# Kernel tuning notes

Measured on AMD Instinct MI355X. Metric: run time of the kernel, lower is better.

The kernel has to match this reference:

```python
import jax, jax.numpy as jnp
import numpy as np
import math

NHEAD = 8
IOU_THR = 0.2
COS_THR = 0.2


def _build_mask(segments, q):
    # segments: [bz, Lq, 2] (center, length); q: [bz, Lq, d]
    c, l = segments[..., 0], segments[..., 1]
    s, e = c - l / 2, c + l / 2  # ml2se: midpoint-length -> start-end
    inter = jnp.clip(jnp.minimum(e[:, :, None], e[:, None, :])
                     - jnp.maximum(s[:, :, None], s[:, None, :]), 0.0)
    union = l[:, :, None] + l[:, None, :] - inter
    iou = inter / union  # [bz, Lq, Lq]
    qn = q / jnp.maximum(jnp.linalg.norm(q, axis=-1, keepdims=True), 1e-8)
    cos = jnp.einsum('bid,bjd->bij', qn, qn)
    Lq = q.shape[1]
    adj = jnp.broadcast_to(jnp.eye(Lq, dtype=bool), iou.shape)
    adj = jnp.where(iou <= IOU_THR, True, adj)   # adj_matrix[iou<=0.2]=1
    adj = jnp.where(cos <= COS_THR, False, adj)  # adj_matrix[cos<=0.2]=0
    return ~adj  # True = masked


def setup_inputs() -> dict:
    key = jax.random.key(0)
    ks = jax.random.split(key, 8)
    Lq, bz, d = 1024, 8, 512
    bound = 1.0 / math.sqrt(d)
    query = jax.random.normal(ks[0], (Lq, bz, d), jnp.float32)
    segments = jax.random.uniform(ks[1], (bz, Lq, 2), jnp.float32)
    Wq = jax.random.uniform(ks[2], (d, d), jnp.float32, -bound, bound)
    bq = jax.random.uniform(ks[3], (d,), jnp.float32, -bound, bound)
    Wk = jax.random.uniform(ks[4], (d, d), jnp.float32, -bound, bound)
    bk = jax.random.uniform(ks[5], (d,), jnp.float32, -bound, bound)
    Wv = jax.random.uniform(ks[6], (d, d), jnp.float32, -bound, bound)
    bv = jax.random.uniform(ks[7], (d,), jnp.float32, -bound, bound)
    return dict(query=query, segments=segments, Wq=Wq, bq=bq, Wk=Wk, bk=bk,
                Wv=Wv, bv=bv)


def reference(query, segments, Wq, bq, Wk, bk, Wv, bv):
    Lq, bz, d = query.shape
    dh = d // NHEAD
    h = jnp.transpose(query, (1, 0, 2))  # [bz, Lq, d]
    mask = _build_mask(segments, h)      # [bz, Lq, Lq], bool
    Q = (h @ Wq.T + bq).reshape(bz, Lq, NHEAD, dh)
    K = (h @ Wk.T + bk).reshape(bz, Lq, NHEAD, dh)
    V = (h @ Wv.T + bv).reshape(bz, Lq, NHEAD, dh)
    scores = jnp.einsum('bihd,bjhd->bhij', Q, K) / math.sqrt(dh)
    scores = jnp.where(mask[:, None, :, :], -jnp.inf, scores)
    attn = jax.nn.softmax(scores, axis=-1)
    out = jnp.einsum('bhij,bjhd->bihd', attn, V).reshape(bz, Lq, d) + h
    return jnp.transpose(out, (1, 0, 2))  # [Lq, bz, d]
```

## Files before the change

### kernel.cpp

```cpp
#include <hip/hip_runtime.h>
#include <math.h>

#define LQ 1024
#define BZ 8
#define D  512
#define NH 8
#define DH 64
#define IOU_THR 0.2f
#define COS_THR 0.2f
#define NEG (-1e30f)
#define FIXCAP 16384

typedef short bf16x8 __attribute__((ext_vector_type(8)));
typedef float f32x4  __attribute__((ext_vector_type(4)));

#define MFMA16(a, b, cacc) __builtin_amdgcn_mfma_f32_16x16x32_bf16(a, b, cacc, 0, 0, 0)

__device__ inline unsigned short f2bf(float x) {
    union { float f; unsigned int u; } v; v.f = x;
    unsigned int r = v.u + 0x7FFF + ((v.u >> 16) & 1);
    return (unsigned short)(r >> 16);
}

__device__ __forceinline__ void gll16(const void* g, void* ldsbase) {
    __builtin_amdgcn_global_load_lds(
        (const __attribute__((address_space(1))) unsigned int*)g,
        (__attribute__((address_space(3))) unsigned int*)ldsbase, 16, 0, 0);
}

__global__ __launch_bounds__(256) void prep_kernel(const float* __restrict__ query,
                                                   float* __restrict__ h,
                                                   unsigned short* __restrict__ hi,
                                                   float* __restrict__ rnorm) {
    int blk = blockIdx.x;
    int b = blk >> 10, i = blk & 1023;
    const float* src = query + ((size_t)i * BZ + b) * D;
    int tid = threadIdx.x;
    float2 v = ((const float2*)src)[tid];
    ((float2*)(h + (size_t)blk * D))[tid] = v;
    unsigned short hx = f2bf(v.x), hy = f2bf(v.y);
    ((unsigned int*)(hi + (size_t)blk * D))[tid] = (unsigned int)hx | ((unsigned int)hy << 16);
    float ss = v.x * v.x + v.y * v.y;
    __shared__ float red[256];
    red[tid] = ss; __syncthreads();
    for (int s = 128; s > 0; s >>= 1) {
        if (tid < s) red[tid] += red[tid + s];
        __syncthreads();
    }
    if (tid == 0) rnorm[blk] = 1.0f / fmaxf(sqrtf(red[0]), 1e-8f);
}

__global__ __launch_bounds__(256) void cvt_w_kernel(const float* __restrict__ Wq,
                                                    const float* __restrict__ Wk,
                                                    const float* __restrict__ Wv,
                                                    unsigned short* __restrict__ Wb) {
    int t = blockIdx.x * 256 + threadIdx.x;
    int mat = t >> 16;
    int off = (t & 65535) * 4;
    const float* src = (mat == 0) ? Wq : (mat == 1) ? Wk : Wv;
    float4 v = *(const float4*)(src + off);
    uint2 p;
    p.x = (unsigned int)f2bf(v.x) | ((unsigned int)f2bf(v.y) << 16);
    p.y = (unsigned int)f2bf(v.z) | ((unsigned int)f2bf(v.w) << 16);
    *(uint2*)(Wb + (size_t)mat * D * D + off) = p;
}

__global__ __launch_bounds__(256) void mask_kernel(const unsigned short* __restrict__ hi,
                                                   const float* __restrict__ rnorm,
                                                   const float* __restrict__ segments,
                                                   unsigned char* __restrict__ mask,
                                                   unsigned char* __restrict__ summ,
                                                   int* __restrict__ fix_cnt,
                                                   unsigned int* __restrict__ fix_list) {
    __shared__ short As[128 * 64], Bs[128 * 64];
    __shared__ float4 iSE[128], jSE[128];
    __shared__ int summ_lds[8][2];
    int b = blockIdx.z, i0 = blockIdx.y * 128, j0 = blockIdx.x * 128;
    int tid = threadIdx.x, w = tid >> 6, lane = tid & 63;
    int c = lane & 15, q4 = lane >> 4;
    int wr = w >> 1, wc = w & 1;
    if (tid < 16) summ_lds[tid >> 1][tid & 1] = 0;

    f32x4 acc[4][4] = {};
    const char* Asrc = (const char*)(hi + ((size_t)b * LQ + i0) * D);
    const char* Bsrc = (const char*)(hi + ((size_t)b * LQ + j0) * D);

    int rgrp = lane >> 3;
    int qg   = (lane & 7) ^ (rgrp & 7);
    size_t lgoff = (size_t)rgrp * 1024 + (size_t)qg * 16;
    int swz = c & 7;

    for (int k0 = 0; k0 < D; k0 += 64) {
        size_t kb = (size_t)k0 * 2;
        #pragma unroll
        for (int m = 0; m < 4; m++) {
            int n = 4 * w + m;
            gll16(Asrc + kb + (size_t)n * 8192 + lgoff, (char*)As + n * 1024);
            gll16(Bsrc + kb + (size_t)n * 8192 + lgoff, (char*)Bs + n * 1024);
        }
        __syncthreads();
        #pragma unroll
        for (int s = 0; s < 2; s++) {
            bf16x8 af[4], bf[4];
            #pragma unroll
            for (int f = 0; f < 4; f++) {
                af[f] = *(const bf16x8*)&As[(wr * 64 + f * 16 + c) * 64 + ((s * 4 + q4) ^ swz) * 8];
                bf[f] = *(const bf16x8*)&Bs[(wc * 64 + f * 16 + c) * 64 + ((s * 4 + q4) ^ swz) * 8];
            }
            #pragma unroll
            for (int fr = 0; fr < 4; fr++)
                #pragma unroll
                for (int fc = 0; fc < 4; fc++)
                    acc[fr][fc] = MFMA16(af[fr], bf[fc], acc[fr][fc]);
        }
        __syncthreads();
    }

    {
        const float2* seg2 = (const float2*)(segments + (size_t)b * LQ * 2);
        const float* rn = rnorm + b * LQ;
        if (tid < 128) {
            int i = i0 + tid;
            float2 cl = seg2[i];
            iSE[tid] = make_float4(cl.x - cl.y * 0.5f, cl.x + cl.y * 0.5f, cl.y, rn[i]);
        } else {
            int j = j0 + tid - 128;
            float2 cl = seg2[j];
            jSE[tid - 128] = make_float4(cl.x - cl.y * 0.5f, cl.x + cl.y * 0.5f, cl.y, rn[j]);
        }
        __syncthreads();
    }

    unsigned char* mbase = mask + ((size_t)b << 20);
    #pragma unroll
    for (int fr = 0; fr < 4; fr++) {
        int anyun = 0;
        #pragma unroll
        for (int r = 0; r < 4; r++) {
            int il = wr * 64 + fr * 16 + q4 * 4 + r;
            int i = i0 + il;
            float4 I = iSE[il];
            #pragma unroll
            for (int fc = 0; fc < 4; fc++) {
                int jl = wc * 64 + fc * 16 + c;
                int j = j0 + jl;
                float4 J = jSE[jl];
                float cosv = acc[fr][fc][r] * I.w * J.w;
                if (fabsf(cosv - COS_THR) < 1.5e-3f) {
                    int idx = atomicAdd(fix_cnt, 1);
                    if (idx < FIXCAP)
                        fix_list[idx] = ((unsigned int)b << 20) | ((unsigned int)i << 10) | j;
                }
                float inter = fmaxf(fminf(I.y, J.y) - fmaxf(I.x, J.x), 0.0f);
                float uni   = I.z + J.z - inter;
                float iou   = inter / uni;
                bool adj = ((iou <= IOU_THR) || (i == j)) && (cosv > COS_THR);
                mbase[(size_t)i * LQ + j] = adj ? 0 : 1;
                anyun |= adj ? 1 : 0;
            }
        }
        if (anyun) atomicOr(&summ_lds[wr * 4 + fr][wc], 1);
    }
    __syncthreads();
    if (tid < 16) {
        int lit = tid >> 1, ljt = tid & 1;
        summ[((size_t)b * 64 + (i0 >> 4) + lit) * 16 + (j0 >> 6) + ljt] =
            summ_lds[lit][ljt] ? 1 : 0;
    }
}

__global__ __launch_bounds__(64) void fixup_kernel(const float* __restrict__ h,
                                                   const float* __restrict__ rnorm,
                                                   const float* __restrict__ segments,
                                                   const int* __restrict__ fix_cnt,
                                                   const unsigned int* __restrict__ fix_list,
                                                   unsigned char* __restrict__ mask,
                                                   unsigned char* __restrict__ summ) {
    int cnt = *fix_cnt; if (cnt > FIXCAP) cnt = FIXCAP;
    int lane = threadIdx.x;
    for (int e = blockIdx.x; e < cnt; e += gridDim.x) {
        unsigned int pk = fix_list[e];
        int b = pk >> 20, i = (pk >> 10) & 1023, j = pk & 1023;
        const float* hri = h + ((size_t)b * LQ + i) * D;
        const float* hrj = h + ((size_t)b * LQ + j) * D;
        double dd = 0.0;
        #pragma unroll
        for (int k = 0; k < D / 64; k++)
            dd += (double)hri[k * 64 + lane] * (double)hrj[k * 64 + lane];
        #pragma unroll
        for (int s = 1; s < 64; s <<= 1) dd += __shfl_xor(dd, s);
        if (lane == 0) {
            float rni = rnorm[b * LQ + i], rnj = rnorm[b * LQ + j];
            float cosv = (float)(dd * (double)rni * (double)rnj);
            const float* seg = segments + (size_t)b * LQ * 2;
            float ci = seg[i * 2], li = seg[i * 2 + 1];
            float cj = seg[j * 2], lj = seg[j * 2 + 1];
            float si = ci - li * 0.5f, ei = ci + li * 0.5f;
            float sj = cj - lj * 0.5f, ej = cj + lj * 0.5f;
            float inter = fmaxf(fminf(ei, ej) - fmaxf(si, sj), 0.0f);
            float iou = inter / (li + lj - inter);
            bool adj = ((iou <= IOU_THR) || (i == j)) && (cosv > COS_THR);
            mask[((size_t)b * LQ + i) * LQ + j] = adj ? 0 : 1;
            if (adj) summ[((size_t)b * 64 + (i >> 4)) * 16 + (j >> 6)] = 1;
        }
    }
}

__global__ __launch_bounds__(256) void qkv_kernel(const unsigned short* __restrict__ hb,
                                                  const unsigned short* __restrict__ Wb,
                                                  const float* __restrict__ bq,
                                                  const float* __restrict__ bk,
                                                  const float* __restrict__ bv,
                                                  unsigned short* __restrict__ Qb,
                                                  unsigned short* __restrict__ Kb,
                                                  unsigned short* __restrict__ Vt) {
    __shared__ short As[128 * 64], Bs[128 * 64];
    int z = blockIdx.z;
    const unsigned short* W = Wb + (size_t)z * D * D;
    const float* bias = (z == 0) ? bq : (z == 1) ? bk : bv;
    int m0 = blockIdx.x * 128, n0 = blockIdx.y * 128;
    int tid = threadIdx.x, w = tid >> 6, lane = tid & 63;
    int c = lane & 15, q4 = lane >> 4;
    int wr = w >> 1, wc = w & 1;

    f32x4 acc[4][4] = {};
    const char* Asrc = (const char*)(hb + (size_t)m0 * D);
    const char* Bsrc = (const char*)(W + (size_t)n0 * D);
    int rgrp = lane >> 3;
    int qg   = (lane & 7) ^ (rgrp & 7);
    size_t lgoff = (size_t)rgrp * 1024 + (size_t)qg * 16;
    int swz = c & 7;

    for (int k0 = 0; k0 < D; k0 += 64) {
        size_t kb = (size_t)k0 * 2;
        #pragma unroll
        for (int m = 0; m < 4; m++) {
            int n = 4 * w + m;
            gll16(Asrc + kb + (size_t)n * 8192 + lgoff, (char*)As + n * 1024);
            gll16(Bsrc + kb + (size_t)n * 8192 + lgoff, (char*)Bs + n * 1024);
        }
        __syncthreads();
        #pragma unroll
        for (int s = 0; s < 2; s++) {
            bf16x8 af[4], bf[4];
            #pragma unroll
            for (int f = 0; f < 4; f++) {
                af[f] = *(const bf16x8*)&As[(wr * 64 + f * 16 + c) * 64 + ((s * 4 + q4) ^ swz) * 8];
                bf[f] = *(const bf16x8*)&Bs[(wc * 64 + f * 16 + c) * 64 + ((s * 4 + q4) ^ swz) * 8];
            }
            #pragma unroll
            for (int fr = 0; fr < 4; fr++)
                #pragma unroll
                for (int fc = 0; fc < 4; fc++)
                    acc[fr][fc] = MFMA16(af[fr], bf[fc], acc[fr][fc]);
        }
        __syncthreads();
    }

    #pragma unroll
    for (int fr = 0; fr < 4; fr++)
        #pragma unroll
        for (int r = 0; r < 4; r++) {
            int m = m0 + wr * 64 + fr * 16 + q4 * 4 + r;
            int b = m >> 10, i = m & 1023;
            #pragma unroll
            for (int fc = 0; fc < 4; fc++) {
                int n = n0 + wc * 64 + fc * 16 + c;
                unsigned short us = f2bf(acc[fr][fc][r] + bias[n]);
                int hh = n >> 6, dh = n & 63;
                size_t bh = (size_t)b * NH + hh;
                if (z == 2)
                    Vt[(bh * DH + dh) * LQ + i] = us;
                else {
                    unsigned short* dst = (z == 0) ? Qb : Kb;
                    dst[(bh * LQ + i) * DH + dh] = us;
                }
            }
        }
}

__global__ __launch_bounds__(256) void attn_kernel(const unsigned short* __restrict__ Qb,
                                                   const unsigned short* __restrict__ Kb,
                                                   const unsigned short* __restrict__ Vt,
                                                   const unsigned char* __restrict__ mask,
                                                   const unsigned char* __restrict__ summ,
                                                   const float* __restrict__ h,
                                                   float* __restrict__ out) {
    int tid = threadIdx.x;
    int w = tid >> 6, lane = tid & 63;
    int c = lane & 15, q4 = lane >> 4;
    int hh = blockIdx.y, b = blockIdx.z;
    int i0 = blockIdx.x * 64 + w * 16;
    size_t bh = (size_t)b * NH + hh;

    __shared__ unsigned short p_lds[4][16][72];

    const unsigned short* Qrow = Qb + (bh * LQ + i0 + c) * DH;
    bf16x8 qa0 = *(const bf16x8*)(Qrow + q4 * 8);
    bf16x8 qa1 = *(const bf16x8*)(Qrow + 32 + q4 * 8);

    f32x4 O[4] = {};
    float m_r[4] = {NEG, NEG, NEG, NEG};
    float l_r[4] = {0.f, 0.f, 0.f, 0.f};

    const unsigned short* Kbase = Kb + bh * LQ * DH;
    const unsigned short* Vbase = Vt + bh * DH * LQ;
    const unsigned char*  mbase = mask + ((size_t)b * LQ + i0) * LQ;
    const unsigned char*  srow  = summ + ((size_t)b * 64 + (i0 >> 4)) * 16;

    for (int jt = 0; jt < 16; jt++) {
        if (!srow[jt]) continue;
        int j0 = jt * 64;
        f32x4 S[4] = {};
        #pragma unroll
        for (int cb = 0; cb < 4; cb++) {
            const unsigned short* krow = Kbase + (size_t)(j0 + cb * 16 + c) * DH;
            bf16x8 kf0 = *(const bf16x8*)(krow + q4 * 8);
            bf16x8 kf1 = *(const bf16x8*)(krow + 32 + q4 * 8);
            S[cb] = MFMA16(qa0, kf0, S[cb]);
            S[cb] = MFMA16(qa1, kf1, S[cb]);
        }
        float p[4][4];
        float tmax[4] = {NEG, NEG, NEG, NEG};
        #pragma unroll
        for (int cb = 0; cb < 4; cb++)
            #pragma unroll
            for (int r = 0; r < 4; r++) {
                float sc = S[cb][r] * 0.125f;
                unsigned char mm = mbase[(size_t)(q4 * 4 + r) * LQ + j0 + cb * 16 + c];
                sc = mm ? NEG : sc;
                p[cb][r] = sc;
                tmax[r] = fmaxf(tmax[r], sc);
            }
        #pragma unroll
        for (int r = 0; r < 4; r++) {
            float v = tmax[r];
            v = fmaxf(v, __shfl_xor(v, 1));
            v = fmaxf(v, __shfl_xor(v, 2));
            v = fmaxf(v, __shfl_xor(v, 4));
            v = fmaxf(v, __shfl_xor(v, 8));
            tmax[r] = v;
        }
        float rsum[4];
        #pragma unroll
        for (int r = 0; r < 4; r++) {
            float mn = fmaxf(m_r[r], tmax[r]);
            float alpha = __expf(m_r[r] - mn);
            m_r[r] = mn;
            l_r[r] *= alpha;
            #pragma unroll
            for (int cb2 = 0; cb2 < 4; cb2++) O[cb2][r] *= alpha;
            float s0 = 0.f;
            #pragma unroll
            for (int cb = 0; cb < 4; cb++) {
                float e = __expf(p[cb][r] - mn);
                p[cb][r] = e;
                s0 += e;
            }
            rsum[r] = s0;
        }
        #pragma unroll
        for (int r = 0; r < 4; r++) {
            float v = rsum[r];
            v += __shfl_xor(v, 1);
            v += __shfl_xor(v, 2);
            v += __shfl_xor(v, 4);
            v += __shfl_xor(v, 8);
            l_r[r] += v;
        }
        #pragma unroll
        for (int cb = 0; cb < 4; cb++)
            #pragma unroll
            for (int r = 0; r < 4; r++)
                p_lds[w][q4 * 4 + r][cb * 16 + c] = f2bf(p[cb][r]);
        #pragma unroll
        for (int s = 0; s < 2; s++) {
            bf16x8 pf = *(const bf16x8*)&p_lds[w][c][s * 32 + q4 * 8];
            #pragma unroll
            for (int cb = 0; cb < 4; cb++) {
                bf16x8 vf = *(const bf16x8*)(Vbase + (size_t)(cb * 16 + c) * LQ + j0 + s * 32 + q4 * 8);
                O[cb] = MFMA16(pf, vf, O[cb]);
            }
        }
    }
    #pragma unroll
    for (int r = 0; r < 4; r++) {
        int i = i0 + q4 * 4 + r;
        float inv = 1.0f / l_r[r];
        #pragma unroll
        for (int cb = 0; cb < 4; cb++) {
            int col = hh * 64 + cb * 16 + c;
            float val = O[cb][r] * inv + h[((size_t)b * LQ + i) * D + col];
            out[((size_t)i * BZ + b) * D + col] = val;
        }
    }
}

extern "C" void kernel_launch(void* const* d_in, const int* in_sizes, int n_in,
                              void* d_out, int out_size, void* d_ws, size_t ws_size,
                              hipStream_t stream) {
    const float* query    = (const float*)d_in[0];
    const float* segments = (const float*)d_in[1];
    const float* Wq = (const float*)d_in[2];
    const float* bq = (const float*)d_in[3];
    const float* Wk = (const float*)d_in[4];
    const float* bk = (const float*)d_in[5];
    const float* Wv = (const float*)d_in[6];
    const float* bv = (const float*)d_in[7];
    float* out = (float*)d_out;

    const size_t NTOK = (size_t)BZ * LQ;
    char* ws = (char*)d_ws;
    float*          h     = (float*)ws;            ws += NTOK * D * 4;
    unsigned short* hbuf  = (unsigned short*)ws;   ws += NTOK * D * 2;
    unsigned short* Qb    = (unsigned short*)ws;   ws += NTOK * D * 2;
    unsigned short* Kb    = (unsigned short*)ws;   ws += NTOK * D * 2;
    unsigned short* Vt    = (unsigned short*)ws;   ws += NTOK * D * 2;
    unsigned short* Wb    = (unsigned short*)ws;   ws += (size_t)3 * D * D * 2;
    float*          rnorm = (float*)ws;            ws += NTOK * 4;
    unsigned char*  mask  = (unsigned char*)ws;    ws += (size_t)BZ * LQ * LQ;
    unsigned char*  summ  = (unsigned char*)ws;    ws += 8192;
    int*            fix_cnt = (int*)ws;            ws += 64;
    unsigned int*   fix_list = (unsigned int*)ws;

    hipMemsetAsync(fix_cnt, 0, 64, stream);
    prep_kernel<<<NTOK, 256, 0, stream>>>(query, h, hbuf, rnorm);
    cvt_w_kernel<<<3 * D * D / 4 / 256, 256, 0, stream>>>(Wq, Wk, Wv, Wb);
    mask_kernel<<<dim3(LQ / 128, LQ / 128, BZ), 256, 0, stream>>>(hbuf, rnorm, segments,
                                                                  mask, summ, fix_cnt, fix_list);
    fixup_kernel<<<64, 64, 0, stream>>>(h, rnorm, segments, fix_cnt, fix_list, mask, summ);
    qkv_kernel<<<dim3(NTOK / 128, D / 128, 3), 256, 0, stream>>>(hbuf, Wb, bq, bk, bv,
                                                                 Qb, Kb, Vt);
    attn_kernel<<<dim3(LQ / 64, NH, BZ), 256, 0, stream>>>(Qb, Kb, Vt, mask, summ, h, out);
}
```

Baseline: 155.7 us.

## Merge prep/weight-convert and mask/QKV GEMMs into combined launches, drop fp32 h copy

Folds query transpose/convert and weight bf16 conversion into one launch, using a wave-per-row layout with shuffle reductions in place of the LDS tree reduction. The mask GEMM and QKV projection GEMM now run as one 1280-block launch, branching on block index. The fp32 transposed copy of h is gone, and the residual and fixup read the original query layout directly. This cuts launch count, kernel-boundary tails and the 16MB of h traffic. The cost is a combined kernel whose two branches may leave register pressure and load imbalance uneven.

Result: slower. 160.5 us (+3.1%).

```diff
diff --git a/kernel.cpp b/kernel.cpp
--- a/kernel.cpp
+++ b/kernel.cpp
@@ -29,67 +29,87 @@
 }
 
 __global__ __launch_bounds__(256) void prep_kernel(const float* __restrict__ query,
-                                                   float* __restrict__ h,
+                                                   const float* __restrict__ Wq,
+                                                   const float* __restrict__ Wk,
+                                                   const float* __restrict__ Wv,
                                                    unsigned short* __restrict__ hi,
+                                                   unsigned short* __restrict__ Wb,
                                                    float* __restrict__ rnorm) {
-    int blk = blockIdx.x;
-    int b = blk >> 10, i = blk & 1023;
-    const float* src = query + ((size_t)i * BZ + b) * D;
-    int tid = threadIdx.x;
-    float2 v = ((const float2*)src)[tid];
-    ((float2*)(h + (size_t)blk * D))[tid] = v;
-    unsigned short hx = f2bf(v.x), hy = f2bf(v.y);
-    ((unsigned int*)(hi + (size_t)blk * D))[tid] = (unsigned int)hx | ((unsigned int)hy << 16);
-    float ss = v.x * v.x + v.y * v.y;
-    __shared__ float red[256];
-    red[tid] = ss; __syncthreads();
-    for (int s = 128; s > 0; s >>= 1) {
-        if (tid < s) red[tid] += red[tid + s];
-        __syncthreads();
-    }
-    if (tid == 0) rnorm[blk] = 1.0f / fmaxf(sqrtf(red[0]), 1e-8f);
-}
-
-__global__ __launch_bounds__(256) void cvt_w_kernel(const float* __restrict__ Wq,
-                                                    const float* __restrict__ Wk,
-                                                    const float* __restrict__ Wv,
-                                                    unsigned short* __restrict__ Wb) {
-    int t = blockIdx.x * 256 + threadIdx.x;
-    int mat = t >> 16;
-    int off = (t & 65535) * 4;
-    const float* src = (mat == 0) ? Wq : (mat == 1) ? Wk : Wv;
-    float4 v = *(const float4*)(src + off);
-    uint2 p;
-    p.x = (unsigned int)f2bf(v.x) | ((unsigned int)f2bf(v.y) << 16);
-    p.y = (unsigned int)f2bf(v.z) | ((unsigned int)f2bf(v.w) << 16);
-    *(uint2*)(Wb + (size_t)mat * D * D + off) = p;
-}
-
-__global__ __launch_bounds__(256) void mask_kernel(const unsigned short* __restrict__ hi,
+    int blk = blockIdx.x, tid = threadIdx.x;
+    if (blk < 2048) {
+        int w = tid >> 6, lane = tid & 63;
+        int row = blk * 4 + w;
+        int b = row >> 10, i = row & 1023;
+        const float* src = query + ((size_t)i * BZ + b) * D + lane * 8;
+        float4 v0 = *(const float4*)src;
+        float4 v1 = *(const float4*)(src + 4);
+        uint4 pk;
+        pk.x = (unsigned)f2bf(v0.x) | ((unsigned)f2bf(v0.y) << 16);
+        pk.y = (unsigned)f2bf(v0.z) | ((unsigned)f2bf(v0.w) << 16);
+        pk.z = (unsigned)f2bf(v1.x) | ((unsigned)f2bf(v1.y) << 16);
+        pk.w = (unsigned)f2bf(v1.z) | ((unsigned)f2bf(v1.w) << 16);
+        *(uint4*)(hi + (size_t)row * D + lane * 8) = pk;
+        float ss = v0.x * v0.x + v0.y * v0.y + v0.z * v0.z + v0.w * v0.w
+                 + v1.x * v1.x + v1.y * v1.y + v1.z * v1.z + v1.w * v1.w;
+        #pragma unroll
+        for (int s = 1; s < 64; s <<= 1) ss += __shfl_xor(ss, s);
+        if (lane == 0) rnorm[row] = 1.0f / fmaxf(sqrtf(ss), 1e-8f);
+    } else {
+        int t = (blk - 2048) * 256 + tid;
+        int mat = t >> 16;
+        int off = (t & 65535) * 4;
+        const float* src = (mat == 0) ? Wq : (mat == 1) ? Wk : Wv;
+        float4 v = *(const float4*)(src + off);
+        uint2 p;
+        p.x = (unsigned)f2bf(v.x) | ((unsigned)f2bf(v.y) << 16);
+        p.y = (unsigned)f2bf(v.z) | ((unsigned)f2bf(v.w) << 16);
+        *(uint2*)(Wb + (size_t)mat * D * D + off) = p;
+    }
+}
+
+__global__ __launch_bounds__(256) void gemm_kernel(const unsigned short* __restrict__ hi,
+                                                   const unsigned short* __restrict__ Wb,
                                                    const float* __restrict__ rnorm,
                                                    const float* __restrict__ segments,
+                                                   const float* __restrict__ bq,
+                                                   const float* __restrict__ bk,
+                                                   const float* __restrict__ bv,
                                                    unsigned char* __restrict__ mask,
                                                    unsigned char* __restrict__ summ,
                                                    int* __restrict__ fix_cnt,
-                                                   unsigned int* __restrict__ fix_list) {
+                                                   unsigned int* __restrict__ fix_list,
+                                                   unsigned short* __restrict__ Qb,
+                                                   unsigned short* __restrict__ Kb,
+                                                   unsigned short* __restrict__ Vt) {
     __shared__ short As[128 * 64], Bs[128 * 64];
     __shared__ float4 iSE[128], jSE[128];
     __shared__ int summ_lds[8][2];
-    int b = blockIdx.z, i0 = blockIdx.y * 128, j0 = blockIdx.x * 128;
-    int tid = threadIdx.x, w = tid >> 6, lane = tid & 63;
+    int blk = blockIdx.x, tid = threadIdx.x, w = tid >> 6, lane = tid & 63;
     int c = lane & 15, q4 = lane >> 4;
     int wr = w >> 1, wc = w & 1;
-    if (tid < 16) summ_lds[tid >> 1][tid & 1] = 0;
-
-    f32x4 acc[4][4] = {};
-    const char* Asrc = (const char*)(hi + ((size_t)b * LQ + i0) * D);
-    const char* Bsrc = (const char*)(hi + ((size_t)b * LQ + j0) * D);
+
+    bool is_qkv = blk < 768;
+    const char *Asrc, *Bsrc;
+    int b = 0, i0 = 0, j0 = 0, z = 0, m0 = 0, n0 = 0;
+    if (is_qkv) {
+        z = blk >> 8; int rem = blk & 255;
+        m0 = (rem >> 2) * 128; n0 = (rem & 3) * 128;
+        Asrc = (const char*)(hi + (size_t)m0 * D);
+        Bsrc = (const char*)(Wb + (size_t)z * D * D + (size_t)n0 * D);
+    } else {
+        int id2 = blk - 768;
+        b = id2 >> 6; i0 = ((id2 >> 3) & 7) * 128; j0 = (id2 & 7) * 128;
+        Asrc = (const char*)(hi + ((size_t)b * LQ + i0) * D);
+        Bsrc = (const char*)(hi + ((size_t)b * LQ + j0) * D);
+        if (tid < 16) summ_lds[tid >> 1][tid & 1] = 0;
+    }
 
     int rgrp = lane >> 3;
     int qg   = (lane & 7) ^ (rgrp & 7);
     size_t lgoff = (size_t)rgrp * 1024 + (size_t)qg * 16;
     int swz = c & 7;
 
+    f32x4 acc[4][4] = {};
     for (int k0 = 0; k0 < D; k0 += 64) {
         size_t kb = (size_t)k0 * 2;
         #pragma unroll
@@ -116,60 +136,80 @@
         __syncthreads();
     }
 
-    {
+    if (is_qkv) {
+        const float* bias = (z == 0) ? bq : (z == 1) ? bk : bv;
+        #pragma unroll
+        for (int fr = 0; fr < 4; fr++)
+            #pragma unroll
+            for (int r = 0; r < 4; r++) {
+                int m = m0 + wr * 64 + fr * 16 + q4 * 4 + r;
+                int bb = m >> 10, i = m & 1023;
+                #pragma unroll
+                for (int fc = 0; fc < 4; fc++) {
+                    int n = n0 + wc * 64 + fc * 16 + c;
+                    unsigned short us = f2bf(acc[fr][fc][r] + bias[n]);
+                    int hh = n >> 6, dh = n & 63;
+                    size_t bh = (size_t)bb * NH + hh;
+                    if (z == 2)
+                        Vt[(bh * DH + dh) * LQ + i] = us;
+                    else {
+                        unsigned short* dst = (z == 0) ? Qb : Kb;
+                        dst[(bh * LQ + i) * DH + dh] = us;
+                    }
+                }
+            }
+    } else {
         const float2* seg2 = (const float2*)(segments + (size_t)b * LQ * 2);
         const float* rn = rnorm + b * LQ;
         if (tid < 128) {
-            int i = i0 + tid;
-            float2 cl = seg2[i];
-            iSE[tid] = make_float4(cl.x - cl.y * 0.5f, cl.x + cl.y * 0.5f, cl.y, rn[i]);
+            float2 cl = seg2[i0 + tid];
+            iSE[tid] = make_float4(cl.x - cl.y * 0.5f, cl.x + cl.y * 0.5f, cl.y, rn[i0 + tid]);
         } else {
-            int j = j0 + tid - 128;
-            float2 cl = seg2[j];
-            jSE[tid - 128] = make_float4(cl.x - cl.y * 0.5f, cl.x + cl.y * 0.5f, cl.y, rn[j]);
+            float2 cl = seg2[j0 + tid - 128];
+            jSE[tid - 128] = make_float4(cl.x - cl.y * 0.5f, cl.x + cl.y * 0.5f, cl.y, rn[j0 + tid - 128]);
         }
         __syncthreads();
-    }
-
-    unsigned char* mbase = mask + ((size_t)b << 20);
-    #pragma unroll
-    for (int fr = 0; fr < 4; fr++) {
-        int anyun = 0;
-        #pragma unroll
-        for (int r = 0; r < 4; r++) {
-            int il = wr * 64 + fr * 16 + q4 * 4 + r;
-            int i = i0 + il;
-            float4 I = iSE[il];
-            #pragma unroll
-            for (int fc = 0; fc < 4; fc++) {
-                int jl = wc * 64 + fc * 16 + c;
-                int j = j0 + jl;
-                float4 J = jSE[jl];
-                float cosv = acc[fr][fc][r] * I.w * J.w;
-                if (fabsf(cosv - COS_THR) < 1.5e-3f) {
-                    int idx = atomicAdd(fix_cnt, 1);
-                    if (idx < FIXCAP)
-                        fix_list[idx] = ((unsigned int)b << 20) | ((unsigned int)i << 10) | j;
+
+        unsigned char* mbase = mask + ((size_t)b << 20);
+        #pragma unroll
+        for (int fr = 0; fr < 4; fr++) {
+            int anyun = 0;
+            #pragma unroll
+            for (int r = 0; r < 4; r++) {
+                int il = wr * 64 + fr * 16 + q4 * 4 + r;
+                int i = i0 + il;
+                float4 I = iSE[il];
+                #pragma unroll
+                for (int fc = 0; fc < 4; fc++) {
+                    int jl = wc * 64 + fc * 16 + c;
+                    int j = j0 + jl;
+                    float4 J = jSE[jl];
+                    float cosv = acc[fr][fc][r] * I.w * J.w;
+                    if (fabsf(cosv - COS_THR) < 1.5e-3f) {
+                        int idx = atomicAdd(fix_cnt, 1);
+                        if (idx < FIXCAP)
+                            fix_list[idx] = ((unsigned int)b << 20) | ((unsigned int)i << 10) | j;
+                    }
+                    float inter = fmaxf(fminf(I.y, J.y) - fmaxf(I.x, J.x), 0.0f);
+                    float uni   = I.z + J.z - inter;
+                    float iou   = inter / uni;
+                    bool adj = ((iou <= IOU_THR) || (i == j)) && (cosv > COS_THR);
+                    mbase[(size_t)i * LQ + j] = adj ? 0 : 1;
+                    anyun |= adj ? 1 : 0;
                 }
-                float inter = fmaxf(fminf(I.y, J.y) - fmaxf(I.x, J.x), 0.0f);
-                float uni   = I.z + J.z - inter;
-                float iou   = inter / uni;
-                bool adj = ((iou <= IOU_THR) || (i == j)) && (cosv > COS_THR);
-                mbase[(size_t)i * LQ + j] = adj ? 0 : 1;
-                anyun |= adj ? 1 : 0;
-            }
-        }
-        if (anyun) atomicOr(&summ_lds[wr * 4 + fr][wc], 1);
-    }
-    __syncthreads();
-    if (tid < 16) {
-        int lit = tid >> 1, ljt = tid & 1;
-        summ[((size_t)b * 64 + (i0 >> 4) + lit) * 16 + (j0 >> 6) + ljt] =
-            summ_lds[lit][ljt] ? 1 : 0;
-    }
-}
-
-__global__ __launch_bounds__(64) void fixup_kernel(const float* __restrict__ h,
+            }
+            if (anyun) atomicOr(&summ_lds[wr * 4 + fr][wc], 1);
+        }
+        __syncthreads();
+        if (tid < 16) {
+            int lit = tid >> 1, ljt = tid & 1;
+            summ[((size_t)b * 64 + (i0 >> 4) + lit) * 16 + (j0 >> 6) + ljt] =
+                summ_lds[lit][ljt] ? 1 : 0;
+        }
+    }
+}
+
+__global__ __launch_bounds__(64) void fixup_kernel(const float* __restrict__ query,
                                                    const float* __restrict__ rnorm,
                                                    const float* __restrict__ segments,
                                                    const int* __restrict__ fix_cnt,
@@ -181,8 +221,8 @@
     for (int e = blockIdx.x; e < cnt; e += gridDim.x) {
         unsigned int pk = fix_list[e];
         int b = pk >> 20, i = (pk >> 10) & 1023, j = pk & 1023;
-        const float* hri = h + ((size_t)b * LQ + i) * D;
-        const float* hrj = h + ((size_t)b * LQ + j) * D;
+        const float* hri = query + ((size_t)i * BZ + b) * D;
+        const float* hrj = query + ((size_t)j * BZ + b) * D;
         double dd = 0.0;
         #pragma unroll
         for (int k = 0; k < D / 64; k++)
@@ -206,85 +246,12 @@
     }
 }
 
-__global__ __launch_bounds__(256) void qkv_kernel(const unsigned short* __restrict__ hb,
-                                                  const unsigned short* __restrict__ Wb,
-                                                  const float* __restrict__ bq,
-                                                  const float* __restrict__ bk,
-                                                  const float* __restrict__ bv,
-                                                  unsigned short* __restrict__ Qb,
-                                                  unsigned short* __restrict__ Kb,
-                                                  unsigned short* __restrict__ Vt) {
-    __shared__ short As[128 * 64], Bs[128 * 64];
-    int z = blockIdx.z;
-    const unsigned short* W = Wb + (size_t)z * D * D;
-    const float* bias = (z == 0) ? bq : (z == 1) ? bk : bv;
-    int m0 = blockIdx.x * 128, n0 = blockIdx.y * 128;
-    int tid = threadIdx.x, w = tid >> 6, lane = tid & 63;
-    int c = lane & 15, q4 = lane >> 4;
-    int wr = w >> 1, wc = w & 1;
-
-    f32x4 acc[4][4] = {};
-    const char* Asrc = (const char*)(hb + (size_t)m0 * D);
-    const char* Bsrc = (const char*)(W + (size_t)n0 * D);
-    int rgrp = lane >> 3;
-    int qg   = (lane & 7) ^ (rgrp & 7);
-    size_t lgoff = (size_t)rgrp * 1024 + (size_t)qg * 16;
-    int swz = c & 7;
-
-    for (int k0 = 0; k0 < D; k0 += 64) {
-        size_t kb = (size_t)k0 * 2;
-        #pragma unroll
-        for (int m = 0; m < 4; m++) {
-            int n = 4 * w + m;
-            gll16(Asrc + kb + (size_t)n * 8192 + lgoff, (char*)As + n * 1024);
-            gll16(Bsrc + kb + (size_t)n * 8192 + lgoff, (char*)Bs + n * 1024);
-        }
-        __syncthreads();
-        #pragma unroll
-        for (int s = 0; s < 2; s++) {
-            bf16x8 af[4], bf[4];
-            #pragma unroll
-            for (int f = 0; f < 4; f++) {
-                af[f] = *(const bf16x8*)&As[(wr * 64 + f * 16 + c) * 64 + ((s * 4 + q4) ^ swz) * 8];
-                bf[f] = *(const bf16x8*)&Bs[(wc * 64 + f * 16 + c) * 64 + ((s * 4 + q4) ^ swz) * 8];
-            }
-            #pragma unroll
-            for (int fr = 0; fr < 4; fr++)
-                #pragma unroll
-                for (int fc = 0; fc < 4; fc++)
-                    acc[fr][fc] = MFMA16(af[fr], bf[fc], acc[fr][fc]);
-        }
-        __syncthreads();
-    }
-
-    #pragma unroll
-    for (int fr = 0; fr < 4; fr++)
-        #pragma unroll
-        for (int r = 0; r < 4; r++) {
-            int m = m0 + wr * 64 + fr * 16 + q4 * 4 + r;
-            int b = m >> 10, i = m & 1023;
-            #pragma unroll
-            for (int fc = 0; fc < 4; fc++) {
-                int n = n0 + wc * 64 + fc * 16 + c;
-                unsigned short us = f2bf(acc[fr][fc][r] + bias[n]);
-                int hh = n >> 6, dh = n & 63;
-                size_t bh = (size_t)b * NH + hh;
-                if (z == 2)
-                    Vt[(bh * DH + dh) * LQ + i] = us;
-                else {
-                    unsigned short* dst = (z == 0) ? Qb : Kb;
-                    dst[(bh * LQ + i) * DH + dh] = us;
-                }
-            }
-        }
-}
-
 __global__ __launch_bounds__(256) void attn_kernel(const unsigned short* __restrict__ Qb,
                                                    const unsigned short* __restrict__ Kb,
                                                    const unsigned short* __restrict__ Vt,
                                                    const unsigned char* __restrict__ mask,
                                                    const unsigned char* __restrict__ summ,
-                                                   const float* __restrict__ h,
+                                                   const float* __restrict__ query,
                                                    float* __restrict__ out) {
     int tid = threadIdx.x;
     int w = tid >> 6, lane = tid & 63;
@@ -390,8 +357,8 @@
         #pragma unroll
         for (int cb = 0; cb < 4; cb++) {
             int col = hh * 64 + cb * 16 + c;
-            float val = O[cb][r] * inv + h[((size_t)b * LQ + i) * D + col];
-            out[((size_t)i * BZ + b) * D + col] = val;
+            size_t oidx = ((size_t)i * BZ + b) * D + col;
+            out[oidx] = O[cb][r] * inv + query[oidx];
         }
     }
 }
@@ -411,7 +378,6 @@
 
     const size_t NTOK = (size_t)BZ * LQ;
     char* ws = (char*)d_ws;
-    float*          h     = (float*)ws;            ws += NTOK * D * 4;
     unsigned short* hbuf  = (unsigned short*)ws;   ws += NTOK * D * 2;
     unsigned short* Qb    = (unsigned short*)ws;   ws += NTOK * D * 2;
     unsigned short* Kb    = (unsigned short*)ws;   ws += NTOK * D * 2;
@@ -424,12 +390,9 @@
     unsigned int*   fix_list = (unsigned int*)ws;
 
     hipMemsetAsync(fix_cnt, 0, 64, stream);
-    prep_kernel<<<NTOK, 256, 0, stream>>>(query, h, hbuf, rnorm);
-    cvt_w_kernel<<<3 * D * D / 4 / 256, 256, 0, stream>>>(Wq, Wk, Wv, Wb);
-    mask_kernel<<<dim3(LQ / 128, LQ / 128, BZ), 256, 0, stream>>>(hbuf, rnorm, segments,
-                                                                  mask, summ, fix_cnt, fix_list);
-    fixup_kernel<<<64, 64, 0, stream>>>(h, rnorm, segments, fix_cnt, fix_list, mask, summ);
-    qkv_kernel<<<dim3(NTOK / 128, D / 128, 3), 256, 0, stream>>>(hbuf, Wb, bq, bk, bv,
-                                                                 Qb, Kb, Vt);
-    attn_kernel<<<dim3(LQ / 64, NH, BZ), 256, 0, stream>>>(Qb, Kb, Vt, mask, summ, h, out);
-}
+    prep_kernel<<<2816, 256, 0, stream>>>(query, Wq, Wk, Wv, hbuf, Wb, rnorm);
+    gemm_kernel<<<1280, 256, 0, stream>>>(hbuf, Wb, rnorm, segments, bq, bk, bv,
+                                          mask, summ, fix_cnt, fix_list, Qb, Kb, Vt);
+    fixup_kernel<<<64, 64, 0, stream>>>(query, rnorm, segments, fix_cnt, fix_list, mask, summ);
+    attn_kernel<<<dim3(LQ / 64, NH, BZ), 256, 0, stream>>>(Qb, Kb, Vt, mask, summ, query, out);
+}
```
